# Optimization experiments

Hardware: AMD Instinct MI355X
Metric: run time of the kernel (lower is better)

## Reference

```python
import jax, jax.numpy as jnp
import numpy as np

B, D, U = 4096, 2048, 2048

def setup_inputs() -> dict:
    key = jax.random.key(0)
    ks = jax.random.split(key, 16)
    s_in = 1.0 / np.sqrt(D)
    s_h = 1.0 / np.sqrt(U)
    inp = {
        "x": jax.random.normal(ks[0], (B, D), jnp.float32),
        "h": jax.random.normal(ks[1], (B, U), jnp.float32),
        "c": jax.random.normal(ks[2], (B, U), jnp.float32),
        # input-to-gate weights (Dense with bias)
        "Wxf": jax.random.normal(ks[3], (D, U), jnp.float32) * s_in,
        "Wxi": jax.random.normal(ks[4], (D, U), jnp.float32) * s_in,
        "Wxo": jax.random.normal(ks[5], (D, U), jnp.float32) * s_in,
        "Wxg": jax.random.normal(ks[6], (D, U), jnp.float32) * s_in,
        "bf": jnp.zeros((U,), jnp.float32),
        "bi": jnp.zeros((U,), jnp.float32),
        "bo": jnp.zeros((U,), jnp.float32),
        "bg": jnp.zeros((U,), jnp.float32),
        # hidden-to-gate weights (no bias)
        "Whf": jax.random.normal(ks[7], (U, U), jnp.float32) * s_h,
        "Whi": jax.random.normal(ks[8], (U, U), jnp.float32) * s_h,
        "Who": jax.random.normal(ks[9], (U, U), jnp.float32) * s_h,
        "Whg": jax.random.normal(ks[10], (U, U), jnp.float32) * s_h,
    }
    return inp

def reference(x, h, c, Wxf, Wxi, Wxo, Wxg, bf, bi, bo, bg, Whf, Whi, Who, Whg):
    # Fuse the 8 small GEMMs into two batched GEMMs over concatenated weights,
    # then one elementwise gate-fusion pass. Math identical to per-Dense form.
    Wx = jnp.concatenate([Wxf, Wxi, Wxo, Wxg], axis=1)   # [D, 4U]
    Wh = jnp.concatenate([Whf, Whi, Who, Whg], axis=1)   # [U, 4U]
    b = jnp.concatenate([bf, bi, bo, bg], axis=0)        # [4U]
    z = x @ Wx + h @ Wh + b                               # [B, 4U]
    zf, zi, zo, zg = jnp.split(z, 4, axis=1)
    f = jax.nn.sigmoid(zf)
    i = jax.nn.sigmoid(zi)
    o = jax.nn.sigmoid(zo)
    g = jnp.tanh(zg)
    c_new = f * c + i * g
    h_new = o * jnp.tanh(c_new)
    return (h_new, c_new)
```

## Files before the change

kernel.cpp:

```cpp
#include <hip/hip_runtime.h>
#include <hip/hip_bf16.h>
#include <stdint.h>

#define B_ 4096
#define D_ 2048
#define U_ 2048
#define K_ 4096
#define N_ 8192

typedef __bf16 bf16x8 __attribute__((ext_vector_type(8)));
typedef float floatx4 __attribute__((ext_vector_type(4)));

__device__ __forceinline__ unsigned short f2bf(float f) {
    union { float f; unsigned int u; } v; v.f = f;
    unsigned int u = v.u;
    unsigned int r = (u + 0x7fffu + ((u >> 16) & 1u)) >> 16;
    return (unsigned short)r;
}

__device__ __forceinline__ float bf2f(unsigned short b) {
    union { unsigned int u; float f; } v;
    v.u = ((unsigned int)b) << 16;
    return v.f;
}

__global__ void k_convA(const float* __restrict__ x, const float* __restrict__ h,
                        unsigned short* __restrict__ Abf) {
    int t = blockIdx.x * blockDim.x + threadIdx.x;
    long e = (long)t * 4;
    int b = (int)(e >> 12);
    int k = (int)(e & 4095);
    const float* src = (k < D_) ? (x + (size_t)b * D_ + k)
                                : (h + (size_t)b * U_ + (k - D_));
    float4 v = *(const float4*)src;
    ushort4 o;
    o.x = f2bf(v.x); o.y = f2bf(v.y); o.z = f2bf(v.z); o.w = f2bf(v.w);
    *(ushort4*)(Abf + e) = o;
}

__global__ void k_convB(const float* __restrict__ Wx0, const float* __restrict__ Wx1,
                        const float* __restrict__ Wx2, const float* __restrict__ Wx3,
                        const float* __restrict__ Wh0, const float* __restrict__ Wh1,
                        const float* __restrict__ Wh2, const float* __restrict__ Wh3,
                        unsigned short* __restrict__ Bt) {
    __shared__ float tile[32][33];
    int g  = blockIdx.z;
    int k0 = blockIdx.x * 32;
    int u0 = blockIdx.y * 32;
    const float* W;
    if (k0 < D_) {
        W = (g == 0 ? Wx0 : g == 1 ? Wx1 : g == 2 ? Wx2 : Wx3) + (size_t)k0 * U_;
    } else {
        W = (g == 0 ? Wh0 : g == 1 ? Wh1 : g == 2 ? Wh2 : Wh3) + (size_t)(k0 - D_) * U_;
    }
    int tx = threadIdx.x & 31, ty = threadIdx.x >> 5;
    #pragma unroll
    for (int j = 0; j < 4; ++j)
        tile[ty + 8 * j][tx] = W[(size_t)(ty + 8 * j) * U_ + u0 + tx];
    __syncthreads();
    #pragma unroll
    for (int j = 0; j < 4; ++j) {
        int u = u0 + ty + 8 * j;
        Bt[(size_t)(g * U_ + u) * K_ + k0 + tx] = f2bf(tile[tx][ty + 8 * j]);
    }
}

__device__ __forceinline__ void gload16(const unsigned short* g, unsigned short* l) {
    __builtin_amdgcn_global_load_lds(
        (const __attribute__((address_space(1))) void*)g,
        (__attribute__((address_space(3))) void*)l, 16, 0, 0);
}

__global__ __launch_bounds__(256) void k_gemm(const unsigned short* __restrict__ A,
                                              const unsigned short* __restrict__ Bt,
                                              unsigned short* __restrict__ Z) {
    __shared__ __align__(16) unsigned short As[128 * 32];
    __shared__ __align__(16) unsigned short Bs[128 * 32];
    const int m0  = blockIdx.y * 128;
    const int n0  = blockIdx.x * 128;
    const int tid = threadIdx.x;
    const int w   = tid >> 6;
    const int l   = tid & 63;

    const unsigned short* gA = A  + (size_t)(m0 + w * 16 + (l >> 2)) * K_ + (l & 3) * 8;
    const unsigned short* gB = Bt + (size_t)(n0 + w * 16 + (l >> 2)) * K_ + (l & 3) * 8;
    unsigned short* lA = As + w * 512;
    unsigned short* lB = Bs + w * 512;

    const int r     = l & 15;
    const int quad  = l >> 4;
    const int m_off = (w & 1) * 64;
    const int n_off = (w >> 1) * 64;

    floatx4 acc[4][4];
    #pragma unroll
    for (int i = 0; i < 4; ++i)
        #pragma unroll
        for (int j = 0; j < 4; ++j)
            #pragma unroll
            for (int e = 0; e < 4; ++e) acc[i][j][e] = 0.f;

    for (int k0 = 0; k0 < K_; k0 += 32) {
        __syncthreads();
        gload16(gA + k0,                  lA);
        gload16(gA + k0 + (size_t)64 * K_, lA + 2048);
        gload16(gB + k0,                  lB);
        gload16(gB + k0 + (size_t)64 * K_, lB + 2048);
        __syncthreads();

        bf16x8 af[4], bfv[4];
        #pragma unroll
        for (int i = 0; i < 4; ++i)
            af[i] = *(const bf16x8*)(As + ((m_off + i * 16 + r) * 32 + quad * 8));
        #pragma unroll
        for (int j = 0; j < 4; ++j)
            bfv[j] = *(const bf16x8*)(Bs + ((n_off + j * 16 + r) * 32 + quad * 8));
        #pragma unroll
        for (int i = 0; i < 4; ++i)
            #pragma unroll
            for (int j = 0; j < 4; ++j)
                acc[i][j] = __builtin_amdgcn_mfma_f32_16x16x32_bf16(
                    af[i], bfv[j], acc[i][j], 0, 0, 0);
    }

    #pragma unroll
    for (int i = 0; i < 4; ++i) {
        #pragma unroll
        for (int j = 0; j < 4; ++j) {
            int col = n0 + n_off + j * 16 + r;
            #pragma unroll
            for (int e = 0; e < 4; ++e) {
                int row = m0 + m_off + i * 16 + quad * 4 + e;
                Z[(size_t)row * N_ + col] = f2bf(acc[i][j][e]);
            }
        }
    }
}

__device__ __forceinline__ float sigmoidf_(float x) { return 1.0f / (1.0f + expf(-x)); }

__global__ void k_gates(const unsigned short* __restrict__ Z, const float* __restrict__ c,
                        const float* __restrict__ bfp, const float* __restrict__ bip,
                        const float* __restrict__ bop, const float* __restrict__ bgp,
                        float* __restrict__ hout, float* __restrict__ cout) {
    int t = blockIdx.x * blockDim.x + threadIdx.x;
    long e = (long)t * 4;
    int b = (int)(e >> 11);
    int u = (int)(e & 2047);
    const size_t zr = (size_t)b * N_;
    ushort4 zf4 = *(const ushort4*)(Z + zr + u);
    ushort4 zi4 = *(const ushort4*)(Z + zr + U_ + u);
    ushort4 zo4 = *(const ushort4*)(Z + zr + 2 * U_ + u);
    ushort4 zg4 = *(const ushort4*)(Z + zr + 3 * U_ + u);
    float4 bfv = *(const float4*)(bfp + u);
    float4 biv = *(const float4*)(bip + u);
    float4 bov = *(const float4*)(bop + u);
    float4 bgv = *(const float4*)(bgp + u);
    float4 cv  = *(const float4*)(c + e);

    float zf[4] = {bf2f(zf4.x), bf2f(zf4.y), bf2f(zf4.z), bf2f(zf4.w)};
    float zi[4] = {bf2f(zi4.x), bf2f(zi4.y), bf2f(zi4.z), bf2f(zi4.w)};
    float zo[4] = {bf2f(zo4.x), bf2f(zo4.y), bf2f(zo4.z), bf2f(zo4.w)};
    float zg[4] = {bf2f(zg4.x), bf2f(zg4.y), bf2f(zg4.z), bf2f(zg4.w)};
    float bff[4] = {bfv.x, bfv.y, bfv.z, bfv.w};
    float bif[4] = {biv.x, biv.y, biv.z, biv.w};
    float bof[4] = {bov.x, bov.y, bov.z, bov.w};
    float bgf[4] = {bgv.x, bgv.y, bgv.z, bgv.w};
    float cf[4]  = {cv.x, cv.y, cv.z, cv.w};

    float4 ho, co;
    float hh[4], cc[4];
    #pragma unroll
    for (int q = 0; q < 4; ++q) {
        float f = sigmoidf_(zf[q] + bff[q]);
        float i = sigmoidf_(zi[q] + bif[q]);
        float o = sigmoidf_(zo[q] + bof[q]);
        float g = tanhf(zg[q] + bgf[q]);
        float cn = f * cf[q] + i * g;
        cc[q] = cn;
        hh[q] = o * tanhf(cn);
    }
    ho.x = hh[0]; ho.y = hh[1]; ho.z = hh[2]; ho.w = hh[3];
    co.x = cc[0]; co.y = cc[1]; co.z = cc[2]; co.w = cc[3];
    *(float4*)(hout + e) = ho;
    *(float4*)(cout + e) = co;
}

extern "C" void kernel_launch(void* const* d_in, const int* in_sizes, int n_in,
                              void* d_out, int out_size, void* d_ws, size_t ws_size,
                              hipStream_t stream) {
    const float* x   = (const float*)d_in[0];
    const float* h   = (const float*)d_in[1];
    const float* c   = (const float*)d_in[2];
    const float* Wxf = (const float*)d_in[3];
    const float* Wxi = (const float*)d_in[4];
    const float* Wxo = (const float*)d_in[5];
    const float* Wxg = (const float*)d_in[6];
    const float* bf  = (const float*)d_in[7];
    const float* bi  = (const float*)d_in[8];
    const float* bo  = (const float*)d_in[9];
    const float* bg  = (const float*)d_in[10];
    const float* Whf = (const float*)d_in[11];
    const float* Whi = (const float*)d_in[12];
    const float* Who = (const float*)d_in[13];
    const float* Whg = (const float*)d_in[14];
    float* out = (float*)d_out;

    unsigned short* Abf = (unsigned short*)d_ws;
    unsigned short* Bt  = Abf + (size_t)B_ * K_;
    unsigned short* Z   = Bt + (size_t)N_ * K_;

    k_convA<<<(B_ * K_ / 4) / 256, 256, 0, stream>>>(x, h, Abf);
    k_convB<<<dim3(K_ / 32, U_ / 32, 4), 256, 0, stream>>>(
        Wxf, Wxi, Wxo, Wxg, Whf, Whi, Who, Whg, Bt);
    k_gemm<<<dim3(N_ / 128, B_ / 128), 256, 0, stream>>>(Abf, Bt, Z);
    k_gates<<<(B_ * U_ / 4) / 256, 256, 0, stream>>>(
        Z, c, bf, bi, bo, bg, out, out + (size_t)B_ * U_);
}
```

Baseline: 593.8 us.

## Fuse LSTM gate epilogue into GEMM via interleaved gate weight layout

Reorders the transposed weight matrix so each 128-column GEMM tile holds 32 units from each of the four gates, which lets the GEMM epilogue apply the sigmoid/tanh gate math and write h and c directly. This removes the bf16 Z intermediate and the separate gates kernel, along with their global memory round trip. The warp tiling changes to 2x8 MFMA tiles per wave, and the transpose kernel moves to 64x64 tiles with vectorized loads and stores. Fast __expf-based activations are used, which slightly change numerics, and the epilogue stores are strided rather than vectorized.

```diff
diff --git a/kernel.cpp b/kernel.cpp
--- a/kernel.cpp
+++ b/kernel.cpp
@@ -10,6 +10,7 @@
 
 typedef __bf16 bf16x8 __attribute__((ext_vector_type(8)));
 typedef float floatx4 __attribute__((ext_vector_type(4)));
+typedef unsigned short ushort8 __attribute__((ext_vector_type(8)));
 
 __device__ __forceinline__ unsigned short f2bf(float f) {
     union { float f; unsigned int u; } v; v.f = f;
@@ -18,10 +19,11 @@
     return (unsigned short)r;
 }
 
-__device__ __forceinline__ float bf2f(unsigned short b) {
-    union { unsigned int u; float f; } v;
-    v.u = ((unsigned int)b) << 16;
-    return v.f;
+__device__ __forceinline__ float sigmoid_(float x) {
+    return 1.0f / (1.0f + __expf(-x));
+}
+__device__ __forceinline__ float tanh_(float x) {
+    return 1.0f - 2.0f / (__expf(2.0f * x) + 1.0f);
 }
 
 __global__ void k_convA(const float* __restrict__ x, const float* __restrict__ h,
@@ -38,30 +40,50 @@
     *(ushort4*)(Abf + e) = o;
 }
 
-__global__ void k_convB(const float* __restrict__ Wx0, const float* __restrict__ Wx1,
-                        const float* __restrict__ Wx2, const float* __restrict__ Wx3,
-                        const float* __restrict__ Wh0, const float* __restrict__ Wh1,
-                        const float* __restrict__ Wh2, const float* __restrict__ Wh3,
-                        unsigned short* __restrict__ Bt) {
-    __shared__ float tile[32][33];
-    int g  = blockIdx.z;
-    int k0 = blockIdx.x * 32;
-    int u0 = blockIdx.y * 32;
+__global__ __launch_bounds__(256) void k_convB(
+        const float* __restrict__ Wx0, const float* __restrict__ Wx1,
+        const float* __restrict__ Wx2, const float* __restrict__ Wx3,
+        const float* __restrict__ Wh0, const float* __restrict__ Wh1,
+        const float* __restrict__ Wh2, const float* __restrict__ Wh3,
+        unsigned short* __restrict__ Bt) {
+    __shared__ float tile[64][65];
+    const int g  = blockIdx.z;
+    const int k0 = blockIdx.x * 64;
+    const int u0 = blockIdx.y * 64;
+    const int t  = threadIdx.x;
     const float* W;
     if (k0 < D_) {
         W = (g == 0 ? Wx0 : g == 1 ? Wx1 : g == 2 ? Wx2 : Wx3) + (size_t)k0 * U_;
     } else {
         W = (g == 0 ? Wh0 : g == 1 ? Wh1 : g == 2 ? Wh2 : Wh3) + (size_t)(k0 - D_) * U_;
     }
-    int tx = threadIdx.x & 31, ty = threadIdx.x >> 5;
-    #pragma unroll
-    for (int j = 0; j < 4; ++j)
-        tile[ty + 8 * j][tx] = W[(size_t)(ty + 8 * j) * U_ + u0 + tx];
+    {
+        const int kr_b = t >> 4;
+        const int uc   = (t & 15) * 4;
+        #pragma unroll
+        for (int p = 0; p < 4; ++p) {
+            int kr = p * 16 + kr_b;
+            float4 v = *(const float4*)(W + (size_t)kr * U_ + u0 + uc);
+            tile[kr][uc + 0] = v.x;
+            tile[kr][uc + 1] = v.y;
+            tile[kr][uc + 2] = v.z;
+            tile[kr][uc + 3] = v.w;
+        }
+    }
     __syncthreads();
-    #pragma unroll
-    for (int j = 0; j < 4; ++j) {
-        int u = u0 + ty + 8 * j;
-        Bt[(size_t)(g * U_ + u) * K_ + k0 + tx] = f2bf(tile[tx][ty + 8 * j]);
+    {
+        const int kc = (t & 7) * 8;
+        #pragma unroll
+        for (int p = 0; p < 2; ++p) {
+            int u_idx = p * 32 + (t >> 3);
+            int u = u0 + u_idx;
+            int nrow = ((u >> 5) << 7) + (g << 5) + (u & 31);
+            ushort8 o;
+            #pragma unroll
+            for (int kk = 0; kk < 8; ++kk)
+                o[kk] = f2bf(tile[kc + kk][u_idx]);
+            *(ushort8*)(Bt + (size_t)nrow * K_ + k0 + kc) = o;
+        }
     }
 }
 
@@ -71,9 +93,12 @@
         (__attribute__((address_space(3))) void*)l, 16, 0, 0);
 }
 
-__global__ __launch_bounds__(256) void k_gemm(const unsigned short* __restrict__ A,
-                                              const unsigned short* __restrict__ Bt,
-                                              unsigned short* __restrict__ Z) {
+__global__ __launch_bounds__(256) void k_gemm(
+        const unsigned short* __restrict__ A, const unsigned short* __restrict__ Bt,
+        const float* __restrict__ cin,
+        const float* __restrict__ bfp, const float* __restrict__ bip,
+        const float* __restrict__ bop, const float* __restrict__ bgp,
+        float* __restrict__ hout, float* __restrict__ cout) {
     __shared__ __align__(16) unsigned short As[128 * 32];
     __shared__ __align__(16) unsigned short Bs[128 * 32];
     const int m0  = blockIdx.y * 128;
@@ -87,103 +112,61 @@
     unsigned short* lA = As + w * 512;
     unsigned short* lB = Bs + w * 512;
 
-    const int r     = l & 15;
-    const int quad  = l >> 4;
-    const int m_off = (w & 1) * 64;
-    const int n_off = (w >> 1) * 64;
-
-    floatx4 acc[4][4];
+    const int r    = l & 15;
+    const int quad = l >> 4;
+
+    floatx4 acc[2][8];
     #pragma unroll
-    for (int i = 0; i < 4; ++i)
-        #pragma unroll
-        for (int j = 0; j < 4; ++j)
+    for (int i = 0; i < 2; ++i)
+        #pragma unroll
+        for (int j = 0; j < 8; ++j)
             #pragma unroll
             for (int e = 0; e < 4; ++e) acc[i][j][e] = 0.f;
 
     for (int k0 = 0; k0 < K_; k0 += 32) {
         __syncthreads();
-        gload16(gA + k0,                  lA);
+        gload16(gA + k0,                   lA);
         gload16(gA + k0 + (size_t)64 * K_, lA + 2048);
-        gload16(gB + k0,                  lB);
+        gload16(gB + k0,                   lB);
         gload16(gB + k0 + (size_t)64 * K_, lB + 2048);
         __syncthreads();
 
-        bf16x8 af[4], bfv[4];
-        #pragma unroll
-        for (int i = 0; i < 4; ++i)
-            af[i] = *(const bf16x8*)(As + ((m_off + i * 16 + r) * 32 + quad * 8));
-        #pragma unroll
-        for (int j = 0; j < 4; ++j)
-            bfv[j] = *(const bf16x8*)(Bs + ((n_off + j * 16 + r) * 32 + quad * 8));
-        #pragma unroll
-        for (int i = 0; i < 4; ++i)
-            #pragma unroll
-            for (int j = 0; j < 4; ++j)
+        bf16x8 af[2], bfv[8];
+        #pragma unroll
+        for (int i = 0; i < 2; ++i)
+            af[i] = *(const bf16x8*)(As + ((w * 32 + i * 16 + r) * 32 + quad * 8));
+        #pragma unroll
+        for (int j = 0; j < 8; ++j)
+            bfv[j] = *(const bf16x8*)(Bs + ((j * 16 + r) * 32 + quad * 8));
+        #pragma unroll
+        for (int i = 0; i < 2; ++i)
+            #pragma unroll
+            for (int j = 0; j < 8; ++j)
                 acc[i][j] = __builtin_amdgcn_mfma_f32_16x16x32_bf16(
                     af[i], bfv[j], acc[i][j], 0, 0, 0);
     }
 
+    const int u_base = (n0 >> 2);
     #pragma unroll
-    for (int i = 0; i < 4; ++i) {
-        #pragma unroll
-        for (int j = 0; j < 4; ++j) {
-            int col = n0 + n_off + j * 16 + r;
+    for (int half = 0; half < 2; ++half) {
+        const int u = u_base + half * 16 + r;
+        const float bfv_ = bfp[u], biv_ = bip[u], bov_ = bop[u], bgv_ = bgp[u];
+        #pragma unroll
+        for (int i = 0; i < 2; ++i) {
             #pragma unroll
             for (int e = 0; e < 4; ++e) {
-                int row = m0 + m_off + i * 16 + quad * 4 + e;
-                Z[(size_t)row * N_ + col] = f2bf(acc[i][j][e]);
+                const int row = m0 + w * 32 + i * 16 + quad * 4 + e;
+                const size_t idx = (size_t)row * U_ + u;
+                float f  = sigmoid_(acc[i][0 + half][e] + bfv_);
+                float ig = sigmoid_(acc[i][2 + half][e] + biv_);
+                float o  = sigmoid_(acc[i][4 + half][e] + bov_);
+                float gg = tanh_   (acc[i][6 + half][e] + bgv_);
+                float cn = f * cin[idx] + ig * gg;
+                cout[idx] = cn;
+                hout[idx] = o * tanh_(cn);
             }
         }
     }
-}
-
-__device__ __forceinline__ float sigmoidf_(float x) { return 1.0f / (1.0f + expf(-x)); }
-
-__global__ void k_gates(const unsigned short* __restrict__ Z, const float* __restrict__ c,
-                        const float* __restrict__ bfp, const float* __restrict__ bip,
-                        const float* __restrict__ bop, const float* __restrict__ bgp,
-                        float* __restrict__ hout, float* __restrict__ cout) {
-    int t = blockIdx.x * blockDim.x + threadIdx.x;
-    long e = (long)t * 4;
-    int b = (int)(e >> 11);
-    int u = (int)(e & 2047);
-    const size_t zr = (size_t)b * N_;
-    ushort4 zf4 = *(const ushort4*)(Z + zr + u);
-    ushort4 zi4 = *(const ushort4*)(Z + zr + U_ + u);
-    ushort4 zo4 = *(const ushort4*)(Z + zr + 2 * U_ + u);
-    ushort4 zg4 = *(const ushort4*)(Z + zr + 3 * U_ + u);
-    float4 bfv = *(const float4*)(bfp + u);
-    float4 biv = *(const float4*)(bip + u);
-    float4 bov = *(const float4*)(bop + u);
-    float4 bgv = *(const float4*)(bgp + u);
-    float4 cv  = *(const float4*)(c + e);
-
-    float zf[4] = {bf2f(zf4.x), bf2f(zf4.y), bf2f(zf4.z), bf2f(zf4.w)};
-    float zi[4] = {bf2f(zi4.x), bf2f(zi4.y), bf2f(zi4.z), bf2f(zi4.w)};
-    float zo[4] = {bf2f(zo4.x), bf2f(zo4.y), bf2f(zo4.z), bf2f(zo4.w)};
-    float zg[4] = {bf2f(zg4.x), bf2f(zg4.y), bf2f(zg4.z), bf2f(zg4.w)};
-    float bff[4] = {bfv.x, bfv.y, bfv.z, bfv.w};
-    float bif[4] = {biv.x, biv.y, biv.z, biv.w};
-    float bof[4] = {bov.x, bov.y, bov.z, bov.w};
-    float bgf[4] = {bgv.x, bgv.y, bgv.z, bgv.w};
-    float cf[4]  = {cv.x, cv.y, cv.z, cv.w};
-
-    float4 ho, co;
-    float hh[4], cc[4];
-    #pragma unroll
-    for (int q = 0; q < 4; ++q) {
-        float f = sigmoidf_(zf[q] + bff[q]);
-        float i = sigmoidf_(zi[q] + bif[q]);
-        float o = sigmoidf_(zo[q] + bof[q]);
-        float g = tanhf(zg[q] + bgf[q]);
-        float cn = f * cf[q] + i * g;
-        cc[q] = cn;
-        hh[q] = o * tanhf(cn);
-    }
-    ho.x = hh[0]; ho.y = hh[1]; ho.z = hh[2]; ho.w = hh[3];
-    co.x = cc[0]; co.y = cc[1]; co.z = cc[2]; co.w = cc[3];
-    *(float4*)(hout + e) = ho;
-    *(float4*)(cout + e) = co;
 }
 
 extern "C" void kernel_launch(void* const* d_in, const int* in_sizes, int n_in,
@@ -208,12 +191,10 @@
 
     unsigned short* Abf = (unsigned short*)d_ws;
     unsigned short* Bt  = Abf + (size_t)B_ * K_;
-    unsigned short* Z   = Bt + (size_t)N_ * K_;
 
     k_convA<<<(B_ * K_ / 4) / 256, 256, 0, stream>>>(x, h, Abf);
-    k_convB<<<dim3(K_ / 32, U_ / 32, 4), 256, 0, stream>>>(
+    k_convB<<<dim3(K_ / 64, U_ / 64, 4), 256, 0, stream>>>(
         Wxf, Wxi, Wxo, Wxg, Whf, Whi, Who, Whg, Bt);
-    k_gemm<<<dim3(N_ / 128, B_ / 128), 256, 0, stream>>>(Abf, Bt, Z);
-    k_gates<<<(B_ * U_ / 4) / 256, 256, 0, stream>>>(
-        Z, c, bf, bi, bo, bg, out, out + (size_t)B_ * U_);
-}
+    k_gemm<<<dim3(N_ / 128, B_ / 128), 256, 0, stream>>>(
+        Abf, Bt, c, bf, bi, bo, bg, out, out + (size_t)B_ * U_);
+}
```

Result: slower. 631.1 us (+6.3%).
